# Performance work log

Measured on AMD Instinct MI355X. Metric: run time of the kernel, lower is better.

## Reference

```python
import jax, jax.numpy as jnp
import numpy as np

B, T, D = 8, 1024, 1024
F, NB, FPB, ES, NE = 64, 4, 16, 4, 16
DFE, DRH, DEH = 128, 256, 512
RIN = D + DFE  # router input dim (hidden + feature embedding)
TEMP = 1.0
BUNDLE_TOPK = 2
EXPERT_TOPK = 2
LN_EPS = 1e-5


def setup_inputs() -> dict:
    key = jax.random.key(0)
    ks = jax.random.split(key, 24)
    s = 0.02
    n = lambda k, shp, sc=s: jax.random.normal(k, shp, dtype=jnp.float32) * sc
    return {
        "hidden": jax.random.normal(ks[0], (B, T, D), dtype=jnp.float32),
        "feat": jax.random.uniform(ks[1], (B, T, F), dtype=jnp.float32),
        "ln_g": jnp.ones((D,), jnp.float32),
        "ln_b": jnp.zeros((D,), jnp.float32),
        "stage_W": n(ks[2], (F, DFE)),
        "stage_b": jnp.zeros((DFE,), jnp.float32),
        "bproj_W": n(ks[3], (NB, FPB, DFE)),
        "bproj_b": jnp.zeros((NB, DFE), jnp.float32),
        "br_W1": n(ks[4], (RIN, DRH)),
        "br_b1": jnp.zeros((DRH,), jnp.float32),
        "br_W2": n(ks[5], (DRH, NB)),
        "br_b2": jnp.zeros((NB,), jnp.float32),
        "ir_W1": n(ks[6], (NB, RIN, DRH)),
        "ir_b1": jnp.zeros((NB, DRH), jnp.float32),
        "ir_W2": n(ks[7], (NB, DRH, ES)),
        "ir_b2": jnp.zeros((NB, ES), jnp.float32),
        "ex_W1": n(ks[8], (NE, D, DEH)),
        "ex_b1": jnp.zeros((NE, DEH), jnp.float32),
        "ex_W2": n(ks[9], (NE, DEH, D)),
        "ex_b2": jnp.zeros((NE, D), jnp.float32),
        "alpha": jnp.float32(1.0),
    }


def _topk_softmax(logits, temp, k):
    # scale by temperature, keep top-k logits, softmax (renormalized over kept)
    s = logits / temp
    if k is not None and k < s.shape[-1]:
        thr = jax.lax.top_k(s, k)[0][..., -1:]
        s = jnp.where(s >= thr, s, -jnp.inf)
    return jax.nn.softmax(s, axis=-1)


def _gelu(x):
    return jax.nn.gelu(x, approximate=False)  # torch nn.GELU default = exact erf


def reference(hidden, feat, ln_g, ln_b, stage_W, stage_b, bproj_W, bproj_b,
              br_W1, br_b1, br_W2, br_b2, ir_W1, ir_b1, ir_W2, ir_b2,
              ex_W1, ex_b1, ex_W2, ex_b2, alpha):
    # pre-LN
    mu = hidden.mean(-1, keepdims=True)
    var = ((hidden - mu) ** 2).mean(-1, keepdims=True)
    h_norm = (hidden - mu) * jax.lax.rsqrt(var + LN_EPS) * ln_g + ln_b  # [B,T,D]

    # stage feature embedding (stage_feat_idx = all 64 features here)
    sfe = feat @ stage_W + stage_b  # [B,T,DFE]
    bundle_in = jnp.concatenate([h_norm, sfe], axis=-1)  # [B,T,RIN]
    bundle_logits = _gelu(bundle_in @ br_W1 + br_b1) @ br_W2 + br_b2  # [B,T,NB]
    bundle_weights = _topk_softmax(bundle_logits, TEMP, BUNDLE_TOPK)

    # intra-bundle routers (vectorized over the 4 bundles)
    # bundle_feat_idx_g = [g*16 .. g*16+15] -> contiguous reshape is exact gather
    bfeat = feat.reshape(B, T, NB, FPB)
    bemb = jnp.einsum('btgf,gfe->btge', bfeat, bproj_W) + bproj_b  # [B,T,NB,DFE]
    iin = jnp.concatenate(
        [jnp.broadcast_to(h_norm[:, :, None, :], (B, T, NB, D)), bemb], axis=-1)
    ih = _gelu(jnp.einsum('btgi,gih->btgh', iin, ir_W1) + ir_b1)
    intra_logits = jnp.einsum('btgh,ghe->btge', ih, ir_W2) + ir_b2  # [B,T,NB,ES]
    intra_weights = _topk_softmax(intra_logits, TEMP, EXPERT_TOPK)

    gate_weights = (bundle_weights[..., None] * intra_weights).reshape(B, T, NE)
    gate_logits = (bundle_logits[..., None] + intra_logits).reshape(B, T, NE)

    # all experts run densely on h_norm, combined by gate weights
    eh = _gelu(jnp.einsum('btd,edh->bteh', h_norm, ex_W1) + ex_b1)  # [B,T,NE,DEH]
    eo = jnp.einsum('bteh,ehd->bted', eh, ex_W2) + ex_b2            # [B,T,NE,D]
    stage_delta = jnp.einsum('bte,bted->btd', gate_weights, eo)

    next_hidden = hidden + alpha * stage_delta  # alpha_scale = 1.0, eval dropout
    return (next_hidden, gate_weights, gate_logits, bundle_weights,
            bundle_logits, stage_delta)
```

## Files before the change

kernel.cpp:

```cpp
#include <hip/hip_runtime.h>


typedef unsigned short u16;
typedef u16 u16x8 __attribute__((ext_vector_type(8)));
typedef __bf16 bf16x8 __attribute__((ext_vector_type(8)));
typedef float f32x4 __attribute__((ext_vector_type(4)));

#define M_TOK 8192

__device__ __forceinline__ float bf2f(u16 u) {
  return __uint_as_float(((unsigned)u) << 16);
}
__device__ __forceinline__ u16 f2bf(float f) {
  unsigned u = __float_as_uint(f);
  unsigned r = (u + 0x7fffu + ((u >> 16) & 1u)) >> 16;
  return (u16)r;
}
__device__ __forceinline__ void split3(float x, u16& p0, u16& p1, u16& p2) {
  p0 = f2bf(x);
  float r = x - bf2f(p0);
  p1 = f2bf(r);
  float r2 = r - bf2f(p1);
  p2 = f2bf(r2);
}
__device__ __forceinline__ float gelu_exact(float x) {
  return 0.5f * x * (1.f + erff(x * 0.70710678118654752f));
}
__device__ __forceinline__ void gload16(const u16* g, u16* l) {
  __builtin_amdgcn_global_load_lds(
      (const __attribute__((address_space(1))) void*)g,
      (__attribute__((address_space(3))) void*)l, 16, 0, 0);
}

#define BAR()                               \
  do {                                      \
    asm volatile("" ::: "memory");          \
    __builtin_amdgcn_s_barrier();           \
    asm volatile("" ::: "memory");          \
  } while (0)
#define WAITV6() asm volatile("s_waitcnt vmcnt(6)" ::: "memory")
#define WAITV0() asm volatile("s_waitcnt vmcnt(0)" ::: "memory")

__global__ void probe_k(int* flag) {
  int lane = threadIdx.x & 63;
  int lq = lane & 15, quad = lane >> 4;
  u16x8 au, bu;
#pragma unroll
  for (int j = 0; j < 8; ++j) {
    int k = quad * 8 + j;
    float av = (k == 0) ? (float)lq : (k == 1 ? 1.f : 0.f);
    float bv = (k == 0) ? 1.f : (k == 1 ? 2.f * (float)lq : 0.f);
    au[j] = f2bf(av);
    bu[j] = f2bf(bv);
  }
  f32x4 acc = {};
  acc = __builtin_amdgcn_mfma_f32_16x16x32_bf16(
      __builtin_bit_cast(bf16x8, au), __builtin_bit_cast(bf16x8, bu), acc, 0, 0, 0);
  bool okg = true, oks = true;
#pragma unroll
  for (int rr = 0; rr < 4; ++rr) {
    float vg = (float)((quad * 4 + rr) + 2 * lq);
    float vs = (float)(lq + 2 * (quad * 4 + rr));
    okg = okg && (acc[rr] == vg);
    oks = oks && (acc[rr] == vs);
  }
  unsigned long long bg = __ballot(okg), bs = __ballot(oks);
  if (threadIdx.x == 0) *flag = (bg == ~0ull) ? 0 : ((bs == ~0ull) ? 1 : 0);
}

__global__ __launch_bounds__(256) void transpose_k(const float* __restrict__ src,
                                                   u16* __restrict__ dst,
                                                   int R, int C) {
  src += (size_t)blockIdx.z * R * C;
  dst += (size_t)blockIdx.z * R * C;
  __shared__ u16 tile[32][33];
  int r0 = blockIdx.x * 32, c0 = blockIdx.y * 32;
  int tx = threadIdx.x, ty = threadIdx.y;
#pragma unroll
  for (int k = 0; k < 4; ++k) {
    int r = r0 + ty + k * 8;
    if (r < R && c0 + tx < C) tile[ty + k * 8][tx] = f2bf(src[(size_t)r * C + c0 + tx]);
  }
  __syncthreads();
#pragma unroll
  for (int k = 0; k < 4; ++k) {
    int c = c0 + ty + k * 8;
    if (c < C && r0 + tx < R) dst[(size_t)c * R + r0 + tx] = tile[tx][ty + k * 8];
  }
}

__global__ __launch_bounds__(256) void transpose_k3(const float* __restrict__ src,
                                                    u16* __restrict__ dst,
                                                    int R, int C, size_t PS) {
  src += (size_t)blockIdx.z * R * C;
  dst += (size_t)blockIdx.z * R * C;
  __shared__ float tile[32][33];
  int r0 = blockIdx.x * 32, c0 = blockIdx.y * 32;
  int tx = threadIdx.x, ty = threadIdx.y;
#pragma unroll
  for (int k = 0; k < 4; ++k) {
    int r = r0 + ty + k * 8;
    if (r < R && c0 + tx < C) tile[ty + k * 8][tx] = src[(size_t)r * C + c0 + tx];
  }
  __syncthreads();
#pragma unroll
  for (int k = 0; k < 4; ++k) {
    int c = c0 + ty + k * 8;
    if (c < C && r0 + tx < R) {
      u16 p0, p1, p2;
      split3(tile[tx][ty + k * 8], p0, p1, p2);
      size_t idx = (size_t)c * R + r0 + tx;
      dst[idx] = p0;
      dst[PS + idx] = p1;
      dst[2 * PS + idx] = p2;
    }
  }
}

__global__ __launch_bounds__(256) void ln_k(const float* __restrict__ h,
                                            const float* __restrict__ gam,
                                            const float* __restrict__ bet,
                                            u16* __restrict__ out) {
  const size_t PS = (size_t)M_TOK * 1024;
  int wave = threadIdx.x >> 6, lane = threadIdx.x & 63;
  int t = blockIdx.x * 4 + wave;
  const float4* row4 = (const float4*)(h + (size_t)t * 1024);
  float x[16];
#pragma unroll
  for (int k = 0; k < 4; ++k) {
    float4 v = row4[lane * 4 + k];
    x[k * 4 + 0] = v.x; x[k * 4 + 1] = v.y; x[k * 4 + 2] = v.z; x[k * 4 + 3] = v.w;
  }
  float s = 0.f, ss = 0.f;
#pragma unroll
  for (int i = 0; i < 16; ++i) { s += x[i]; ss += x[i] * x[i]; }
#pragma unroll
  for (int m = 1; m < 64; m <<= 1) { s += __shfl_xor(s, m); ss += __shfl_xor(ss, m); }
  float mu = s * (1.f / 1024.f);
  float var = ss * (1.f / 1024.f) - mu * mu;
  float inv = rsqrtf(var + 1e-5f);
  const float4* g4 = (const float4*)gam;
  const float4* b4 = (const float4*)bet;
  u16x8 o0[3], o1[3];
#pragma unroll
  for (int k = 0; k < 4; ++k) {
    float4 g = g4[lane * 4 + k];
    float4 b = b4[lane * 4 + k];
    float vals[4] = {(x[k * 4 + 0] - mu) * inv * g.x + b.x,
                     (x[k * 4 + 1] - mu) * inv * g.y + b.y,
                     (x[k * 4 + 2] - mu) * inv * g.z + b.z,
                     (x[k * 4 + 3] - mu) * inv * g.w + b.w};
#pragma unroll
    for (int e = 0; e < 4; ++e) {
      u16 p0, p1, p2;
      split3(vals[e], p0, p1, p2);
      int sl = k * 4 + e;
      if (sl < 8) { o0[0][sl] = p0; o0[1][sl] = p1; o0[2][sl] = p2; }
      else { o1[0][sl - 8] = p0; o1[1][sl - 8] = p1; o1[2][sl - 8] = p2; }
    }
  }
  size_t base = (size_t)t * 1024 + lane * 16;
#pragma unroll
  for (int p = 0; p < 3; ++p) {
    *(u16x8*)(out + p * PS + base) = o0[p];
    *(u16x8*)(out + p * PS + base + 8) = o1[p];
  }
}

__global__ __launch_bounds__(128) void feat_k(const float* __restrict__ feat,
    const float* __restrict__ stW, const float* __restrict__ stb,
    const float* __restrict__ bpW, const float* __restrict__ bpb,
    u16* __restrict__ sfe3, u16* __restrict__ bemb3) {
  const size_t S_PS = (size_t)M_TOK * 128;
  const size_t E_PS = (size_t)4 * M_TOK * 128;
  int t = blockIdx.x;
  int n = threadIdx.x;
  __shared__ float fsh[64];
  if (n < 64) fsh[n] = feat[(size_t)t * 64 + n];
  __syncthreads();
  float s = stb[n];
  for (int k = 0; k < 64; ++k) s += fsh[k] * stW[k * 128 + n];
  {
    u16 p0, p1, p2;
    split3(s, p0, p1, p2);
    size_t idx = (size_t)t * 128 + n;
    sfe3[idx] = p0; sfe3[S_PS + idx] = p1; sfe3[2 * S_PS + idx] = p2;
  }
#pragma unroll
  for (int g = 0; g < 4; ++g) {
    float v = bpb[g * 128 + n];
#pragma unroll
    for (int j = 0; j < 16; ++j)
      v += fsh[g * 16 + j] * bpW[(g * 16 + j) * 128 + n];
    u16 p0, p1, p2;
    split3(v, p0, p1, p2);
    size_t idx = ((size_t)g * M_TOK + t) * 128 + n;
    bemb3[idx] = p0; bemb3[E_PS + idx] = p1; bemb3[2 * E_PS + idx] = p2;
  }
}

__global__ __launch_bounds__(256) void rgemm_k(
    const u16* __restrict__ hn3, const u16* __restrict__ sfe3,
    const u16* __restrict__ bemb3, const u16* __restrict__ Bt3,
    const float* __restrict__ bias0, const float* __restrict__ bias1,
    float* __restrict__ ih, const int* __restrict__ flagp) {
  __shared__ __align__(16) u16 shA[3][64 * 64];
  __shared__ __align__(16) u16 shB[3][64 * 64];
  const int tid = threadIdx.x;
  const int wave = tid >> 6, lane = tid & 63;
  const int gz = blockIdx.x >> 2;
  const int bn64 = (blockIdx.x & 3) * 64;
  const int bm64 = blockIdx.y * 64;
  const size_t A_PS = (size_t)M_TOK * 1024;
  const size_t S_PS = (size_t)M_TOK * 128;
  const size_t E_PS = (size_t)4 * M_TOK * 128;
  const size_t B_PS = (size_t)5 * 256 * 1152;
  const u16* AexB = (gz == 0) ? sfe3 : (bemb3 + (size_t)(gz - 1) * M_TOK * 128);
  const size_t Aex_PS = (gz == 0) ? S_PS : E_PS;
  const u16* BtP = Bt3 + (size_t)gz * 256 * 1152;

  f32x4 acc[2][2] = {};
  const int lq = lane & 15, quad = lane >> 4;
  const int wm = (wave >> 1) * 32, wn = (wave & 1) * 32;

  for (int kit = 0; kit < 18; ++kit) {
    int k0 = kit * 64;
#pragma unroll
    for (int half = 0; half < 2; ++half) {
      int ch = half * 256 + tid;
      int r = ch >> 3, ssl = ch & 7;
      int c = ssl ^ (r & 7);
      int gk = k0 + c * 8;
#pragma unroll
      for (int p = 0; p < 3; ++p) {
        const u16* gA = (gk < 1024)
            ? (hn3 + (size_t)p * A_PS + (size_t)(bm64 + r) * 1024 + gk)
            : (AexB + (size_t)p * Aex_PS + (size_t)(bm64 + r) * 128 + (gk - 1024));
        const u16* gB = BtP + (size_t)p * B_PS + (size_t)(bn64 + r) * 1152 + gk;
        gload16(gA, &shA[p][(half * 256 + wave * 64) * 8]);
        gload16(gB, &shB[p][(half * 256 + wave * 64) * 8]);
      }
    }
    __syncthreads();
#pragma unroll
    for (int ks = 0; ks < 2; ++ks) {
      bf16x8 af[3][2], bfr[3][2];
#pragma unroll
      for (int i = 0; i < 2; ++i) {
        int r = wm + i * 16 + lq;
        int cc = (ks * 4 + quad) ^ (r & 7);
        int rb = wn + i * 16 + lq;
        int cb = (ks * 4 + quad) ^ (rb & 7);
#pragma unroll
        for (int p = 0; p < 3; ++p) {
          af[p][i] = *(const bf16x8*)&shA[p][(r * 8 + cc) * 8];
          bfr[p][i] = *(const bf16x8*)&shB[p][(rb * 8 + cb) * 8];
        }
      }
#pragma unroll
      for (int i = 0; i < 2; ++i)
#pragma unroll
        for (int j = 0; j < 2; ++j) {
          acc[i][j] = __builtin_amdgcn_mfma_f32_16x16x32_bf16(af[0][i], bfr[0][j], acc[i][j], 0, 0, 0);
          acc[i][j] = __builtin_amdgcn_mfma_f32_16x16x32_bf16(af[0][i], bfr[1][j], acc[i][j], 0, 0, 0);
          acc[i][j] = __builtin_amdgcn_mfma_f32_16x16x32_bf16(af[1][i], bfr[0][j], acc[i][j], 0, 0, 0);
          acc[i][j] = __builtin_amdgcn_mfma_f32_16x16x32_bf16(af[0][i], bfr[2][j], acc[i][j], 0, 0, 0);
          acc[i][j] = __builtin_amdgcn_mfma_f32_16x16x32_bf16(af[1][i], bfr[1][j], acc[i][j], 0, 0, 0);
          acc[i][j] = __builtin_amdgcn_mfma_f32_16x16x32_bf16(af[2][i], bfr[0][j], acc[i][j], 0, 0, 0);
        }
    }
    __syncthreads();
  }

  const int fl = *flagp;
  const float* biasP = (gz == 0) ? bias0 : (bias1 + (gz - 1) * 256);
#pragma unroll
  for (int i = 0; i < 2; ++i) {
#pragma unroll
    for (int j = 0; j < 2; ++j) {
#pragma unroll
      for (int rr = 0; rr < 4; ++rr) {
        int m, col;
        if (fl == 0) {
          m = bm64 + wm + i * 16 + quad * 4 + rr;
          col = bn64 + wn + j * 16 + lq;
        } else {
          m = bm64 + wm + i * 16 + lq;
          col = bn64 + wn + j * 16 + quad * 4 + rr;
        }
        ih[((size_t)gz * M_TOK + m) * 256 + col] = gelu_exact(acc[i][j][rr] + biasP[col]);
      }
    }
  }
}

__global__ __launch_bounds__(512, 2) void ffn1_k(
    const u16* __restrict__ A0, const u16* __restrict__ Bt0,
    const float* __restrict__ b1all, const float* __restrict__ gwf,
    u16* __restrict__ out16, int e0, const int* __restrict__ flagp) {
  __shared__ __align__(16) u16 ldsA[2][2][128 * 64];
  __shared__ __align__(16) u16 ldsB[2][2][128 * 64];
  const int tid = threadIdx.x;
  const int wid = tid >> 6, lane = tid & 63;
  const int lq = lane & 15, quad = lane >> 4;
  const int swz = lq & 7;
  const int wmb = (wid >> 2) * 64;
  const int wnb = (wid & 3) * 32;
  const int ez = blockIdx.x >> 1;
  const int bn = (blockIdx.x & 1) * 256;
  const int bm = blockIdx.y * 256;
  const u16* BtP = Bt0 + (size_t)ez * 512 * 1024;

  f32x4 acc[8][4] = {};
  bf16x8 af[4][2], bfr[4][2];

  auto stageA = [&](int tt, int h) {
#pragma unroll
    for (int q = 0; q < 2; ++q) {
      int ch = q * 512 + tid;
      int r = ch >> 3, ssl = ch & 7;
      int c = ssl ^ (r & 7);
      gload16(A0 + (size_t)(bm + h * 128 + r) * 1024 + tt * 64 + c * 8,
              &ldsA[tt & 1][h][(q * 512 + (tid & ~63)) * 8]);
    }
  };
  auto stageB = [&](int tt, int h) {
#pragma unroll
    for (int q = 0; q < 2; ++q) {
      int ch = q * 512 + tid;
      int r = ch >> 3, ssl = ch & 7;
      int c = ssl ^ (r & 7);
      gload16(BtP + (size_t)(bn + h * 128 + r) * 1024 + tt * 64 + c * 8,
              &ldsB[tt & 1][h][(q * 512 + (tid & ~63)) * 8]);
    }
  };

  stageA(0, 0); stageB(0, 0); stageB(0, 1); stageA(0, 1);
  stageA(1, 0); stageB(1, 0); stageB(1, 1);
  WAITV6();
  BAR();

#pragma unroll 2
  for (int t = 0; t < 16; ++t) {
    const int buf = t & 1;
#pragma unroll
    for (int i = 0; i < 4; ++i) {
      int rh = wmb + i * 16 + lq;
#pragma unroll
      for (int ks = 0; ks < 2; ++ks)
        af[i][ks] = *(const bf16x8*)&ldsA[buf][0][(rh * 8 + ((ks * 4 + quad) ^ swz)) * 8];
    }
#pragma unroll
    for (int g = 0; g < 4; ++g) {
      int rh = wnb + (g & 1) * 16 + lq;
#pragma unroll
      for (int ks = 0; ks < 2; ++ks)
        bfr[g][ks] = *(const bf16x8*)&ldsB[buf][g >> 1][(rh * 8 + ((ks * 4 + quad) ^ swz)) * 8];
    }
    if (t + 1 < 16) stageA(t + 1, 1);
    BAR();
    __builtin_amdgcn_s_setprio(1);
#pragma unroll
    for (int i = 0; i < 4; ++i)
#pragma unroll
      for (int g = 0; g < 2; ++g) {
        acc[i][g] = __builtin_amdgcn_mfma_f32_16x16x32_bf16(af[i][0], bfr[g][0], acc[i][g], 0, 0, 0);
        acc[i][g] = __builtin_amdgcn_mfma_f32_16x16x32_bf16(af[i][1], bfr[g][1], acc[i][g], 0, 0, 0);
      }
    __builtin_amdgcn_s_setprio(0);
    BAR();
    if (t + 2 < 16) stageA(t + 2, 0);
    BAR();
    __builtin_amdgcn_s_setprio(1);
#pragma unroll
    for (int i = 0; i < 4; ++i)
#pragma unroll
      for (int g = 2; g < 4; ++g) {
        acc[i][g] = __builtin_amdgcn_mfma_f32_16x16x32_bf16(af[i][0], bfr[g][0], acc[i][g], 0, 0, 0);
        acc[i][g] = __builtin_amdgcn_mfma_f32_16x16x32_bf16(af[i][1], bfr[g][1], acc[i][g], 0, 0, 0);
      }
    __builtin_amdgcn_s_setprio(0);
    BAR();
#pragma unroll
    for (int i = 0; i < 4; ++i) {
      int rh = wmb + i * 16 + lq;
#pragma unroll
      for (int ks = 0; ks < 2; ++ks)
        af[i][ks] = *(const bf16x8*)&ldsA[buf][1][(rh * 8 + ((ks * 4 + quad) ^ swz)) * 8];
    }
    if (t + 2 < 16) stageB(t + 2, 0);
    BAR();
    __builtin_amdgcn_s_setprio(1);
#pragma unroll
    for (int i = 0; i < 4; ++i)
#pragma unroll
      for (int g = 0; g < 2; ++g) {
        acc[4 + i][g] = __builtin_amdgcn_mfma_f32_16x16x32_bf16(af[i][0], bfr[g][0], acc[4 + i][g], 0, 0, 0);
        acc[4 + i][g] = __builtin_amdgcn_mfma_f32_16x16x32_bf16(af[i][1], bfr[g][1], acc[4 + i][g], 0, 0, 0);
      }
    __builtin_amdgcn_s_setprio(0);
    BAR();
    if (t + 2 < 16) stageB(t + 2, 1);
    BAR();
    __builtin_amdgcn_s_setprio(1);
#pragma unroll
    for (int i = 0; i < 4; ++i)
#pragma unroll
      for (int g = 2; g < 4; ++g) {
        acc[4 + i][g] = __builtin_amdgcn_mfma_f32_16x16x32_bf16(af[i][0], bfr[g][0], acc[4 + i][g], 0, 0, 0);
        acc[4 + i][g] = __builtin_amdgcn_mfma_f32_16x16x32_bf16(af[i][1], bfr[g][1], acc[4 + i][g], 0, 0, 0);
      }
    __builtin_amdgcn_s_setprio(0);
    if (t == 14) { WAITV0(); } else { WAITV6(); }
    BAR();
  }

  const int fl = *flagp;
  const float* biasP = b1all + (e0 + ez) * 512;
#pragma unroll
  for (int f = 0; f < 8; ++f) {
    int mbase = bm + wmb + (f & 3) * 16 + (f >> 2) * 128;
#pragma unroll
    for (int g = 0; g < 4; ++g) {
      int cbase = bn + wnb + (g & 1) * 16 + (g >> 1) * 128;
#pragma unroll
      for (int rr = 0; rr < 4; ++rr) {
        int m, col;
        if (fl == 0) {
          m = mbase + quad * 4 + rr;
          col = cbase + lq;
        } else {
          m = mbase + lq;
          col = cbase + quad * 4 + rr;
        }
        float w = gwf[(size_t)m * 16 + e0 + ez];
        out16[((size_t)ez * M_TOK + m) * 512 + col] =
            f2bf(w * gelu_exact(acc[f][g][rr] + biasP[col]));
      }
    }
  }
}

template <int MODE>
__global__ __launch_bounds__(256) void gemm128_k(
    const u16* __restrict__ A0, const u16* __restrict__ Bt0,
    const float* __restrict__ bias0, const float* __restrict__ gwf,
    float* __restrict__ out32, u16* __restrict__ out16,
    int e0, int first, const int* __restrict__ flagp) {
  __shared__ __align__(16) u16 shA[128 * 64];
  __shared__ __align__(16) u16 shB[128 * 64];
  const int tid = threadIdx.x;
  const int wave = tid >> 6, lane = tid & 63;
  int bm, bn, ez = 0;
  if constexpr (MODE == 1) {
    ez = blockIdx.x & 7;
    bn = (blockIdx.x >> 3) * 128;
  } else {
    bn = blockIdx.x * 128;
  }
  bm = blockIdx.y * 128;

  const u16* BtP;
  int KITER;
  if constexpr (MODE == 1) {
    BtP = Bt0 + (size_t)ez * 512 * 1024;
    KITER = 16;
  } else {
    BtP = Bt0;
    KITER = 64;
  }

  f32x4 acc[4][4] = {};
  const int lq = lane & 15, quad = lane >> 4;
  const int wr = (wave >> 1) * 64, wc = (wave & 1) * 64;

  for (int kit = 0; kit < KITER; ++kit) {
    int k0 = kit * 64;
#pragma unroll
    for (int q = 0; q < 4; ++q) {
      int ch = q * 256 + tid;
      int r = ch >> 3, ssl = ch & 7;
      int c = ssl ^ (r & 7);
      int gk = k0 + c * 8;
      const u16 *gA, *gB;
      if constexpr (MODE == 1) {
        gA = A0 + (size_t)(bm + r) * 1024 + gk;
        gB = BtP + (size_t)(bn + r) * 1024 + gk;
      } else {
        int el = gk >> 9, kk = gk & 511;
        gA = A0 + ((size_t)el * M_TOK + bm + r) * 512 + kk;
        gB = BtP + ((size_t)el * 1024 + bn + r) * 512 + kk;
      }
      gload16(gA, &shA[(q * 256 + wave * 64) * 8]);
      gload16(gB, &shB[(q * 256 + wave * 64) * 8]);
    }
    __syncthreads();
#pragma unroll
    for (int ks = 0; ks < 2; ++ks) {
      bf16x8 af[4], bfr[4];
#pragma unroll
      for (int i = 0; i < 4; ++i) {
        int r = wr + i * 16 + lq;
        int cc = (ks * 4 + quad) ^ (r & 7);
        af[i] = *(const bf16x8*)&shA[(r * 8 + cc) * 8];
        int rb = wc + i * 16 + lq;
        int cb = (ks * 4 + quad) ^ (rb & 7);
        bfr[i] = *(const bf16x8*)&shB[(rb * 8 + cb) * 8];
      }
#pragma unroll
      for (int i = 0; i < 4; ++i)
#pragma unroll
        for (int j = 0; j < 4; ++j)
          acc[i][j] = __builtin_amdgcn_mfma_f32_16x16x32_bf16(af[i], bfr[j], acc[i][j], 0, 0, 0);
    }
    __syncthreads();
  }

  const int fl = *flagp;
  const float* biasP = nullptr;
  if constexpr (MODE == 1) biasP = bias0 + (e0 + ez) * 512;

#pragma unroll
  for (int i = 0; i < 4; ++i) {
#pragma unroll
    for (int j = 0; j < 4; ++j) {
#pragma unroll
      for (int rr = 0; rr < 4; ++rr) {
        int m, col;
        if (fl == 0) {
          m = bm + wr + i * 16 + quad * 4 + rr;
          col = bn + wc + j * 16 + lq;
        } else {
          m = bm + wr + i * 16 + lq;
          col = bn + wc + j * 16 + quad * 4 + rr;
        }
        float v = acc[i][j][rr];
        if constexpr (MODE == 1) {
          float w = gwf[(size_t)m * 16 + e0 + ez];
          out16[((size_t)ez * M_TOK + m) * 512 + col] =
              f2bf(w * gelu_exact(v + biasP[col]));
        } else {
          size_t idx = (size_t)m * 1024 + col;
          float prev = first ? 0.f : out32[idx];
          out32[idx] = prev + v;
        }
      }
    }
  }
}

__device__ __forceinline__ void topk2_softmax4(const float* s, float* w) {
  float m1 = fmaxf(fmaxf(s[0], s[1]), fmaxf(s[2], s[3]));
  float m2 = -1e30f;
  bool seen = false;
#pragma unroll
  for (int i = 0; i < 4; ++i) {
    if (s[i] == m1 && !seen) seen = true;
    else m2 = fmaxf(m2, s[i]);
  }
  float e[4];
  float sum = 0.f;
#pragma unroll
  for (int i = 0; i < 4; ++i) {
    e[i] = (s[i] >= m2) ? expf(s[i] - m1) : 0.f;
    sum += e[i];
  }
  float invs = 1.f / sum;
#pragma unroll
  for (int i = 0; i < 4; ++i) w[i] = e[i] * invs;
}

__global__ __launch_bounds__(256) void gating_k(
    const float* __restrict__ ih_all, const float* __restrict__ brW2,
    const float* __restrict__ brb2, const float* __restrict__ irW2,
    const float* __restrict__ irb2, float* __restrict__ gwf,
    float* __restrict__ o_gw, float* __restrict__ o_gl,
    float* __restrict__ o_bw, float* __restrict__ o_bl) {
  int wave = threadIdx.x >> 6, lane = threadIdx.x & 63;
  int t = blockIdx.x * 4 + wave;
  const float4* bw4 = (const float4*)brW2;
  const float4* iw4 = (const float4*)irW2;
  float v[20];
#pragma unroll
  for (int i = 0; i < 20; ++i) v[i] = 0.f;
  const float* bh = ih_all + (size_t)t * 256;
#pragma unroll
  for (int jj = 0; jj < 4; ++jj) {
    int k = jj * 64 + lane;
    float h = bh[k];
    float4 wv = bw4[k];
    v[0] += h * wv.x; v[1] += h * wv.y; v[2] += h * wv.z; v[3] += h * wv.w;
  }
#pragma unroll
  for (int g = 0; g < 4; ++g) {
    const float* ihg = ih_all + ((size_t)(1 + g) * M_TOK + t) * 256;
#pragma unroll
    for (int jj = 0; jj < 4; ++jj) {
      int k = jj * 64 + lane;
      float h = ihg[k];
      float4 wv = iw4[g * 256 + k];
      v[4 + g * 4 + 0] += h * wv.x; v[4 + g * 4 + 1] += h * wv.y;
      v[4 + g * 4 + 2] += h * wv.z; v[4 + g * 4 + 3] += h * wv.w;
    }
  }
#pragma unroll
  for (int i = 0; i < 20; ++i)
#pragma unroll
    for (int m = 1; m < 64; m <<= 1) v[i] += __shfl_xor(v[i], m);
  if (lane == 0) {
    float blog[4], ilog[4][4];
#pragma unroll
    for (int c = 0; c < 4; ++c) blog[c] = v[c] + brb2[c];
#pragma unroll
    for (int g = 0; g < 4; ++g)
#pragma unroll
      for (int e = 0; e < 4; ++e) ilog[g][e] = v[4 + g * 4 + e] + irb2[g * 4 + e];
    float bw[4];
    topk2_softmax4(blog, bw);
#pragma unroll
    for (int g = 0; g < 4; ++g) {
      float iw[4];
      topk2_softmax4(ilog[g], iw);
#pragma unroll
      for (int e = 0; e < 4; ++e) {
        int idx = g * 4 + e;
        float wv = bw[g] * iw[e];
        gwf[(size_t)t * 16 + idx] = wv;
        o_gw[(size_t)t * 16 + idx] = wv;
        o_gl[(size_t)t * 16 + idx] = blog[g] + ilog[g][e];
      }
      o_bw[(size_t)t * 4 + g] = bw[g];
      o_bl[(size_t)t * 4 + g] = blog[g];
    }
  }
}

__global__ __launch_bounds__(256) void combine_k(
    const float* __restrict__ gwf, const float* __restrict__ b2,
    const float* __restrict__ hidden, const float* __restrict__ alpha_p,
    float* __restrict__ o_next, float* __restrict__ o_delta) {
  int row = blockIdx.x;
  float a = alpha_p[0];
  float wb[16];
#pragma unroll
  for (int e = 0; e < 16; ++e) wb[e] = gwf[(size_t)row * 16 + e];
#pragma unroll
  for (int k = 0; k < 4; ++k) {
    int c = threadIdx.x + k * 256;
    float s = 0.f;
#pragma unroll
    for (int e = 0; e < 16; ++e) s += wb[e] * b2[e * 1024 + c];
    size_t idx = (size_t)row * 1024 + c;
    float d = o_delta[idx] + s;
    o_delta[idx] = d;
    o_next[idx] = hidden[idx] + a * d;
  }
}

extern "C" void kernel_launch(void* const* d_in, const int* in_sizes, int n_in,
                              void* d_out, int out_size, void* d_ws, size_t ws_size,
                              hipStream_t stream) {
  (void)in_sizes; (void)n_in; (void)out_size; (void)ws_size;
  const float* hidden  = (const float*)d_in[0];
  const float* feat    = (const float*)d_in[1];
  const float* ln_g    = (const float*)d_in[2];
  const float* ln_b    = (const float*)d_in[3];
  const float* stage_W = (const float*)d_in[4];
  const float* stage_b = (const float*)d_in[5];
  const float* bproj_W = (const float*)d_in[6];
  const float* bproj_b = (const float*)d_in[7];
  const float* br_W1   = (const float*)d_in[8];
  const float* br_b1   = (const float*)d_in[9];
  const float* br_W2   = (const float*)d_in[10];
  const float* br_b2   = (const float*)d_in[11];
  const float* ir_W1   = (const float*)d_in[12];
  const float* ir_b1   = (const float*)d_in[13];
  const float* ir_W2   = (const float*)d_in[14];
  const float* ir_b2   = (const float*)d_in[15];
  const float* ex_W1   = (const float*)d_in[16];
  const float* ex_b1   = (const float*)d_in[17];
  const float* ex_W2   = (const float*)d_in[18];
  const float* ex_b2   = (const float*)d_in[19];
  const float* alpha   = (const float*)d_in[20];

  char* w = (char*)d_ws;
  size_t off = 0;
  auto alloc = [&](size_t bytes) {
    void* p = w + off;
    off += (bytes + 255) & ~(size_t)255;
    return p;
  };
  int* flagp   = (int*)alloc(256);
  u16* wt3     = (u16*)alloc(3ull * 5 * 256 * 1152 * 2);
  u16* hn3     = (u16*)alloc(3ull * M_TOK * 1024 * 2);
  float* gwf   = (float*)alloc((size_t)M_TOK * 16 * 4);
  char* region = (char*)alloc(88090000);
  u16* sfe3   = (u16*)region;
  u16* bemb3  = (u16*)(region + 6291456);
  float* ih   = (float*)(region + 6291456 + 25165824);
  u16* w1t_g  = (u16*)region;
  u16* w2t_g  = (u16*)(region + 8388608);
  u16* Gbuf   = (u16*)(region + 16777216);

  float* out = (float*)d_out;
  float* o_next  = out;
  float* o_gw    = out + 8388608;
  float* o_gl    = o_gw + 131072;
  float* o_bw    = o_gl + 131072;
  float* o_bl    = o_bw + 32768;
  float* o_delta = o_bl + 32768;

  probe_k<<<1, 64, 0, stream>>>(flagp);

  transpose_k3<<<dim3(36, 8, 1), dim3(32, 8), 0, stream>>>(
      br_W1, wt3, 1152, 256, (size_t)5 * 256 * 1152);
  transpose_k3<<<dim3(36, 8, 4), dim3(32, 8), 0, stream>>>(
      ir_W1, wt3 + 256 * 1152, 1152, 256, (size_t)5 * 256 * 1152);

  ln_k<<<2048, 256, 0, stream>>>(hidden, ln_g, ln_b, hn3);
  feat_k<<<8192, 128, 0, stream>>>(feat, stage_W, stage_b, bproj_W, bproj_b, sfe3, bemb3);

  rgemm_k<<<dim3(20, 128), 256, 0, stream>>>(hn3, sfe3, bemb3, wt3, br_b1, ir_b1, ih, flagp);
  gating_k<<<2048, 256, 0, stream>>>(ih, br_W2, br_b2, ir_W2, ir_b2, gwf,
                                     o_gw, o_gl, o_bw, o_bl);

  for (int grp = 0; grp < 2; ++grp) {
    transpose_k<<<dim3(32, 16, 8), dim3(32, 8), 0, stream>>>(
        ex_W1 + (size_t)grp * 8 * 1024 * 512, w1t_g, 1024, 512);
    transpose_k<<<dim3(16, 32, 8), dim3(32, 8), 0, stream>>>(
        ex_W2 + (size_t)grp * 8 * 512 * 1024, w2t_g, 512, 1024);
    ffn1_k<<<dim3(16, 32), 512, 0, stream>>>(hn3, w1t_g, ex_b1, gwf,
                                             Gbuf, grp * 8, flagp);
    gemm128_k<2><<<dim3(8, 64), 256, 0, stream>>>(Gbuf, w2t_g, nullptr, nullptr,
                                                  o_delta, nullptr, grp * 8,
                                                  grp == 0 ? 1 : 0, flagp);
  }

  combine_k<<<8192, 256, 0, stream>>>(gwf, ex_b2, hidden, alpha, o_next, o_delta);
}
```

Before: 850.4 us.

## Replace FFN2 GEMM with 256x256 double-buffered split-K pipelined kernel

Replaces the 128x128 single-buffered FFN2 GEMM with a 512-thread 256x256-tile kernel. It double-buffers LDS, interleaves async global loads with MFMA phases, and raises wave priority during the MFMA phases. The K dimension across the 8 experts is split in two: one half accumulates into o_delta and the other into a scratch partial buffer placed inside unused workspace, which combine_k then sums. This aims to raise data reuse and overlap loads with compute. The cost is extra partial-buffer traffic and heavy LDS and register use.

```diff
diff --git a/kernel.cpp b/kernel.cpp
--- a/kernel.cpp
+++ b/kernel.cpp
@@ -441,109 +441,149 @@
   }
 }
 
-template <int MODE>
-__global__ __launch_bounds__(256) void gemm128_k(
+__global__ __launch_bounds__(512, 2) void ffn2_k(
     const u16* __restrict__ A0, const u16* __restrict__ Bt0,
-    const float* __restrict__ bias0, const float* __restrict__ gwf,
-    float* __restrict__ out32, u16* __restrict__ out16,
-    int e0, int first, const int* __restrict__ flagp) {
-  __shared__ __align__(16) u16 shA[128 * 64];
-  __shared__ __align__(16) u16 shB[128 * 64];
+    float* __restrict__ outD, float* __restrict__ outP,
+    int first, const int* __restrict__ flagp) {
+  __shared__ __align__(16) u16 ldsA[2][2][128 * 64];
+  __shared__ __align__(16) u16 ldsB[2][2][128 * 64];
   const int tid = threadIdx.x;
-  const int wave = tid >> 6, lane = tid & 63;
-  int bm, bn, ez = 0;
-  if constexpr (MODE == 1) {
-    ez = blockIdx.x & 7;
-    bn = (blockIdx.x >> 3) * 128;
-  } else {
-    bn = blockIdx.x * 128;
-  }
-  bm = blockIdx.y * 128;
-
-  const u16* BtP;
-  int KITER;
-  if constexpr (MODE == 1) {
-    BtP = Bt0 + (size_t)ez * 512 * 1024;
-    KITER = 16;
-  } else {
-    BtP = Bt0;
-    KITER = 64;
-  }
-
-  f32x4 acc[4][4] = {};
+  const int wid = tid >> 6, lane = tid & 63;
   const int lq = lane & 15, quad = lane >> 4;
-  const int wr = (wave >> 1) * 64, wc = (wave & 1) * 64;
-
-  for (int kit = 0; kit < KITER; ++kit) {
-    int k0 = kit * 64;
-#pragma unroll
-    for (int q = 0; q < 4; ++q) {
-      int ch = q * 256 + tid;
+  const int swz = lq & 7;
+  const int wmb = (wid >> 2) * 64;
+  const int wnb = (wid & 3) * 32;
+  const int kz = blockIdx.x & 1;
+  const int bn = (blockIdx.x >> 1) * 256;
+  const int bm = blockIdx.y * 256;
+
+  f32x4 acc[8][4] = {};
+  bf16x8 af[4][2], bfr[4][2];
+
+  auto stageA = [&](int tt, int h) {
+#pragma unroll
+    for (int q = 0; q < 2; ++q) {
+      int ch = q * 512 + tid;
       int r = ch >> 3, ssl = ch & 7;
       int c = ssl ^ (r & 7);
-      int gk = k0 + c * 8;
-      const u16 *gA, *gB;
-      if constexpr (MODE == 1) {
-        gA = A0 + (size_t)(bm + r) * 1024 + gk;
-        gB = BtP + (size_t)(bn + r) * 1024 + gk;
-      } else {
-        int el = gk >> 9, kk = gk & 511;
-        gA = A0 + ((size_t)el * M_TOK + bm + r) * 512 + kk;
-        gB = BtP + ((size_t)el * 1024 + bn + r) * 512 + kk;
-      }
-      gload16(gA, &shA[(q * 256 + wave * 64) * 8]);
-      gload16(gB, &shB[(q * 256 + wave * 64) * 8]);
-    }
-    __syncthreads();
-#pragma unroll
-    for (int ks = 0; ks < 2; ++ks) {
-      bf16x8 af[4], bfr[4];
-#pragma unroll
-      for (int i = 0; i < 4; ++i) {
-        int r = wr + i * 16 + lq;
-        int cc = (ks * 4 + quad) ^ (r & 7);
-        af[i] = *(const bf16x8*)&shA[(r * 8 + cc) * 8];
-        int rb = wc + i * 16 + lq;
-        int cb = (ks * 4 + quad) ^ (rb & 7);
-        bfr[i] = *(const bf16x8*)&shB[(rb * 8 + cb) * 8];
-      }
-#pragma unroll
-      for (int i = 0; i < 4; ++i)
-#pragma unroll
-        for (int j = 0; j < 4; ++j)
-          acc[i][j] = __builtin_amdgcn_mfma_f32_16x16x32_bf16(af[i], bfr[j], acc[i][j], 0, 0, 0);
-    }
-    __syncthreads();
+      int el = kz * 4 + (tt >> 3), kk = (tt & 7) * 64 + c * 8;
+      gload16(A0 + ((size_t)el * M_TOK + bm + h * 128 + r) * 512 + kk,
+              &ldsA[tt & 1][h][(q * 512 + (tid & ~63)) * 8]);
+    }
+  };
+  auto stageB = [&](int tt, int h) {
+#pragma unroll
+    for (int q = 0; q < 2; ++q) {
+      int ch = q * 512 + tid;
+      int r = ch >> 3, ssl = ch & 7;
+      int c = ssl ^ (r & 7);
+      int el = kz * 4 + (tt >> 3), kk = (tt & 7) * 64 + c * 8;
+      gload16(Bt0 + ((size_t)el * 1024 + bn + h * 128 + r) * 512 + kk,
+              &ldsB[tt & 1][h][(q * 512 + (tid & ~63)) * 8]);
+    }
+  };
+
+  stageA(0, 0); stageB(0, 0); stageB(0, 1); stageA(0, 1);
+  stageA(1, 0); stageB(1, 0); stageB(1, 1);
+  WAITV6();
+  BAR();
+
+#pragma unroll 2
+  for (int t = 0; t < 32; ++t) {
+    const int buf = t & 1;
+#pragma unroll
+    for (int i = 0; i < 4; ++i) {
+      int rh = wmb + i * 16 + lq;
+#pragma unroll
+      for (int ks = 0; ks < 2; ++ks)
+        af[i][ks] = *(const bf16x8*)&ldsA[buf][0][(rh * 8 + ((ks * 4 + quad) ^ swz)) * 8];
+    }
+#pragma unroll
+    for (int g = 0; g < 4; ++g) {
+      int rh = wnb + (g & 1) * 16 + lq;
+#pragma unroll
+      for (int ks = 0; ks < 2; ++ks)
+        bfr[g][ks] = *(const bf16x8*)&ldsB[buf][g >> 1][(rh * 8 + ((ks * 4 + quad) ^ swz)) * 8];
+    }
+    if (t + 1 < 32) stageA(t + 1, 1);
+    BAR();
+    __builtin_amdgcn_s_setprio(1);
+#pragma unroll
+    for (int i = 0; i < 4; ++i)
+#pragma unroll
+      for (int g = 0; g < 2; ++g) {
+        acc[i][g] = __builtin_amdgcn_mfma_f32_16x16x32_bf16(af[i][0], bfr[g][0], acc[i][g], 0, 0, 0);
+        acc[i][g] = __builtin_amdgcn_mfma_f32_16x16x32_bf16(af[i][1], bfr[g][1], acc[i][g], 0, 0, 0);
+      }
+    __builtin_amdgcn_s_setprio(0);
+    BAR();
+    if (t + 2 < 32) stageA(t + 2, 0);
+    BAR();
+    __builtin_amdgcn_s_setprio(1);
+#pragma unroll
+    for (int i = 0; i < 4; ++i)
+#pragma unroll
+      for (int g = 2; g < 4; ++g) {
+        acc[i][g] = __builtin_amdgcn_mfma_f32_16x16x32_bf16(af[i][0], bfr[g][0], acc[i][g], 0, 0, 0);
+        acc[i][g] = __builtin_amdgcn_mfma_f32_16x16x32_bf16(af[i][1], bfr[g][1], acc[i][g], 0, 0, 0);
+      }
+    __builtin_amdgcn_s_setprio(0);
+    BAR();
+#pragma unroll
+    for (int i = 0; i < 4; ++i) {
+      int rh = wmb + i * 16 + lq;
+#pragma unroll
+      for (int ks = 0; ks < 2; ++ks)
+        af[i][ks] = *(const bf16x8*)&ldsA[buf][1][(rh * 8 + ((ks * 4 + quad) ^ swz)) * 8];
+    }
+    if (t + 2 < 32) stageB(t + 2, 0);
+    BAR();
+    __builtin_amdgcn_s_setprio(1);
+#pragma unroll
+    for (int i = 0; i < 4; ++i)
+#pragma unroll
+      for (int g = 0; g < 2; ++g) {
+        acc[4 + i][g] = __builtin_amdgcn_mfma_f32_16x16x32_bf16(af[i][0], bfr[g][0], acc[4 + i][g], 0, 0, 0);
+        acc[4 + i][g] = __builtin_amdgcn_mfma_f32_16x16x32_bf16(af[i][1], bfr[g][1], acc[4 + i][g], 0, 0, 0);
+      }
+    __builtin_amdgcn_s_setprio(0);
+    BAR();
+    if (t + 2 < 32) stageB(t + 2, 1);
+    BAR();
+    __builtin_amdgcn_s_setprio(1);
+#pragma unroll
+    for (int i = 0; i < 4; ++i)
+#pragma unroll
+      for (int g = 2; g < 4; ++g) {
+        acc[4 + i][g] = __builtin_amdgcn_mfma_f32_16x16x32_bf16(af[i][0], bfr[g][0], acc[4 + i][g], 0, 0, 0);
+        acc[4 + i][g] = __builtin_amdgcn_mfma_f32_16x16x32_bf16(af[i][1], bfr[g][1], acc[4 + i][g], 0, 0, 0);
+      }
+    __builtin_amdgcn_s_setprio(0);
+    if (t == 30) { WAITV0(); } else { WAITV6(); }
+    BAR();
   }
 
   const int fl = *flagp;
-  const float* biasP = nullptr;
-  if constexpr (MODE == 1) biasP = bias0 + (e0 + ez) * 512;
-
-#pragma unroll
-  for (int i = 0; i < 4; ++i) {
-#pragma unroll
-    for (int j = 0; j < 4; ++j) {
+  float* outp = kz ? outP : outD;
+#pragma unroll
+  for (int f = 0; f < 8; ++f) {
+    int mbase = bm + wmb + (f & 3) * 16 + (f >> 2) * 128;
+#pragma unroll
+    for (int g = 0; g < 4; ++g) {
+      int cbase = bn + wnb + (g & 1) * 16 + (g >> 1) * 128;
 #pragma unroll
       for (int rr = 0; rr < 4; ++rr) {
         int m, col;
         if (fl == 0) {
-          m = bm + wr + i * 16 + quad * 4 + rr;
-          col = bn + wc + j * 16 + lq;
+          m = mbase + quad * 4 + rr;
+          col = cbase + lq;
         } else {
-          m = bm + wr + i * 16 + lq;
-          col = bn + wc + j * 16 + quad * 4 + rr;
+          m = mbase + lq;
+          col = cbase + quad * 4 + rr;
         }
-        float v = acc[i][j][rr];
-        if constexpr (MODE == 1) {
-          float w = gwf[(size_t)m * 16 + e0 + ez];
-          out16[((size_t)ez * M_TOK + m) * 512 + col] =
-              f2bf(w * gelu_exact(v + biasP[col]));
-        } else {
-          size_t idx = (size_t)m * 1024 + col;
-          float prev = first ? 0.f : out32[idx];
-          out32[idx] = prev + v;
-        }
+        size_t idx = (size_t)m * 1024 + col;
+        float v = acc[f][g][rr];
+        outp[idx] = first ? v : (outp[idx] + v);
       }
     }
   }
@@ -638,6 +678,7 @@
 __global__ __launch_bounds__(256) void combine_k(
     const float* __restrict__ gwf, const float* __restrict__ b2,
     const float* __restrict__ hidden, const float* __restrict__ alpha_p,
+    const float* __restrict__ part,
     float* __restrict__ o_next, float* __restrict__ o_delta) {
   int row = blockIdx.x;
   float a = alpha_p[0];
@@ -651,7 +692,7 @@
 #pragma unroll
     for (int e = 0; e < 16; ++e) s += wb[e] * b2[e * 1024 + c];
     size_t idx = (size_t)row * 1024 + c;
-    float d = o_delta[idx] + s;
+    float d = o_delta[idx] + part[idx] + s;
     o_delta[idx] = d;
     o_next[idx] = hidden[idx] + a * d;
   }
@@ -701,6 +742,7 @@
   u16* w1t_g  = (u16*)region;
   u16* w2t_g  = (u16*)(region + 8388608);
   u16* Gbuf   = (u16*)(region + 16777216);
+  float* o_part1 = (float*)(((char*)hn3) + (size_t)M_TOK * 1024 * 2);
 
   float* out = (float*)d_out;
   float* o_next  = out;
@@ -731,10 +773,10 @@
         ex_W2 + (size_t)grp * 8 * 512 * 1024, w2t_g, 512, 1024);
     ffn1_k<<<dim3(16, 32), 512, 0, stream>>>(hn3, w1t_g, ex_b1, gwf,
                                              Gbuf, grp * 8, flagp);
-    gemm128_k<2><<<dim3(8, 64), 256, 0, stream>>>(Gbuf, w2t_g, nullptr, nullptr,
-                                                  o_delta, nullptr, grp * 8,
-                                                  grp == 0 ? 1 : 0, flagp);
-  }
-
-  combine_k<<<8192, 256, 0, stream>>>(gwf, ex_b2, hidden, alpha, o_next, o_delta);
-}
+    ffn2_k<<<dim3(8, 32), 512, 0, stream>>>(Gbuf, w2t_g, o_delta, o_part1,
+                                            grp == 0 ? 1 : 0, flagp);
+  }
+
+  combine_k<<<8192, 256, 0, stream>>>(gwf, ex_b2, hidden, alpha, o_part1,
+                                      o_next, o_delta);
+}
```

Measured after the change: 813.5 us. 4.3% less time.
